# Optimization experiments

Hardware: AMD Instinct MI355X
Metric: run time of the kernel (lower is better)

Reference implementation:

```python
import jax, jax.numpy as jnp
import numpy as np

N_MESH, N_GRID, N_EDGE = 2562, 16384, 49152
D, EDGE_DIM, OUT_DIM = 512, 4, 128
LN_EPS = 1e-5


def _mlp_ln(x, w1, b1, w2, b2, g, beta):
    # Linear -> ReLU -> Linear -> LayerNorm (activate_final=False, use_layer_norm=True)
    h = jax.nn.relu(x @ w1 + b1)
    h = h @ w2 + b2
    mu = jnp.mean(h, axis=-1, keepdims=True)
    var = jnp.var(h, axis=-1, keepdims=True)
    return (h - mu) * jax.lax.rsqrt(var + LN_EPS) * g + beta


def setup_inputs() -> dict:
    key = jax.random.key(0)
    ks = iter(jax.random.split(key, 40))

    def W(i, o):
        return (jax.random.normal(next(ks), (i, o), jnp.float32) / np.float32(np.sqrt(i)))

    inp = {
        "input_mesh_nodes": jax.random.normal(next(ks), (N_MESH, D), jnp.float32),
        "input_grid_nodes": jax.random.normal(next(ks), (N_GRID, D), jnp.float32),
        "input_edge_attr": jax.random.normal(next(ks), (N_EDGE, EDGE_DIM), jnp.float32),
        "edge_index": jnp.stack([
            jax.random.randint(next(ks), (N_EDGE,), 0, N_MESH, jnp.int32),  # senders (mesh)
            jax.random.randint(next(ks), (N_EDGE,), 0, N_GRID, jnp.int32),  # receivers (grid)
        ], axis=0),
        # edges_mlp: EDGE_DIM -> D -> D, LN
        "emlp_w1": W(EDGE_DIM, D), "emlp_b1": jnp.zeros((D,), jnp.float32),
        "emlp_w2": W(D, D), "emlp_b2": jnp.zeros((D,), jnp.float32),
        "emlp_g": jnp.ones((D,), jnp.float32), "emlp_beta": jnp.zeros((D,), jnp.float32),
        # gnn message MLP: 3D -> D -> D, LN   (cat(x_i, x_j, edge_attr))
        "ge_w1": W(3 * D, D), "ge_b1": jnp.zeros((D,), jnp.float32),
        "ge_w2": W(D, D), "ge_b2": jnp.zeros((D,), jnp.float32),
        "ge_g": jnp.ones((D,), jnp.float32), "ge_beta": jnp.zeros((D,), jnp.float32),
        # gnn node MLP: 2D -> D -> D, LN   (cat(receiver_x, aggr))
        "gn_w1": W(2 * D, D), "gn_b1": jnp.zeros((D,), jnp.float32),
        "gn_w2": W(D, D), "gn_b2": jnp.zeros((D,), jnp.float32),
        "gn_g": jnp.ones((D,), jnp.float32), "gn_beta": jnp.zeros((D,), jnp.float32),
        # grid_mlp_final: D -> D -> OUT_DIM, LN
        "fin_w1": W(D, D), "fin_b1": jnp.zeros((D,), jnp.float32),
        "fin_w2": W(D, OUT_DIM), "fin_b2": jnp.zeros((OUT_DIM,), jnp.float32),
        "fin_g": jnp.ones((OUT_DIM,), jnp.float32), "fin_beta": jnp.zeros((OUT_DIM,), jnp.float32),
    }
    return inp


def reference(input_mesh_nodes, input_grid_nodes, input_edge_attr, edge_index,
              emlp_w1, emlp_b1, emlp_w2, emlp_b2, emlp_g, emlp_beta,
              ge_w1, ge_b1, ge_w2, ge_b2, ge_g, ge_beta,
              gn_w1, gn_b1, gn_w2, gn_b2, gn_g, gn_beta,
              fin_w1, fin_b1, fin_w2, fin_b2, fin_g, fin_beta):
    # edge embedding MLP
    edges_emb = _mlp_ln(input_edge_attr, emlp_w1, emlp_b1, emlp_w2, emlp_b2, emlp_g, emlp_beta)
    senders, receivers = edge_index[0], edge_index[1]
    x_i = input_grid_nodes[receivers]   # receiver (grid) features gathered per edge
    x_j = input_mesh_nodes[senders]     # sender (mesh) features gathered per edge
    # per-edge message MLP on cat(x_i, x_j, edge_attr)
    msg = _mlp_ln(jnp.concatenate([x_i, x_j, edges_emb], axis=-1),
                  ge_w1, ge_b1, ge_w2, ge_b2, ge_g, ge_beta)  # [E, D]
    # scatter-add messages to receiver grid nodes (aggr='add')
    aggr = jax.ops.segment_sum(msg, receivers, num_segments=N_GRID)  # [N_GRID, D]
    # node update MLP on cat(receiver_x, aggr)
    gnn_out = _mlp_ln(jnp.concatenate([input_grid_nodes, aggr], axis=-1),
                      gn_w1, gn_b1, gn_w2, gn_b2, gn_g, gn_beta)
    latent_grid_nodes = input_grid_nodes + gnn_out  # residual
    return _mlp_ln(latent_grid_nodes, fin_w1, fin_b1, fin_w2, fin_b2, fin_g, fin_beta)
```

## Files before the change

### kernel.cpp

```cpp
#include <hip/hip_runtime.h>
#include <hip/hip_bf16.h>
#include <stdint.h>

#define LN_EPS 1e-5f

typedef __hip_bfloat16 bf16;
typedef short short8 __attribute__((ext_vector_type(8)));
typedef float f32x4 __attribute__((ext_vector_type(4)));

static __device__ __forceinline__ float bf2f(short s) {
    unsigned int u = ((unsigned int)(unsigned short)s) << 16;
    return __uint_as_float(u);
}
static __device__ __forceinline__ short f2bf(float x) {
    __hip_bfloat16 h = __float2bfloat16(x);
    return *reinterpret_cast<short*>(&h);
}

static __device__ __forceinline__ void gload16(const void* g, void* l) {
    __builtin_amdgcn_global_load_lds((const __attribute__((address_space(1))) void*)g,
                                     (__attribute__((address_space(3))) void*)l, 16, 0, 0);
}

struct TDesc { const float* src; bf16* dst; int K; int N; int kOff; const float* scale; };
struct TDescs { TDesc d[9]; };

__global__ void transpose_all_kernel(TDescs descs) {
    TDesc t = descs.d[blockIdx.z];
    int kb = blockIdx.x * 32, nb = blockIdx.y * 32;
    if (kb >= t.K || nb >= t.N) return;
    __shared__ float tile[32][33];
    int tx = threadIdx.x & 31, ty = threadIdx.x >> 5;
    for (int i = ty; i < 32; i += 8) {
        int k = kb + i, n = nb + tx;
        float v = (k < t.K && n < t.N) ? t.src[(size_t)(t.kOff + k) * t.N + n] : 0.f;
        if (t.scale && k < t.K) v *= t.scale[k];
        tile[i][tx] = v;
    }
    __syncthreads();
    for (int i = ty; i < 32; i += 8) {
        int n = nb + i, k = kb + tx;
        if (n < t.N && k < t.K)
            t.dst[(size_t)n * t.K + k] = __float2bfloat16(tile[tx][i]);
    }
}

__global__ void uv_kernel(const float* __restrict__ W, const float* __restrict__ g,
                          const float* __restrict__ be, float* __restrict__ u,
                          float* __restrict__ v) {
    int n = blockIdx.x * 256 + threadIdx.x;
    if (n >= 512) return;
    float su = 0.f, sv = 0.f;
    for (int k = 0; k < 512; k++) {
        float w = W[(size_t)(1024 + k) * 512 + n];
        su += g[k] * w;
        sv += be[k] * w;
    }
    u[n] = su;
    v[n] = sv;
}

__global__ void cvt_bf16_kernel(const float* __restrict__ src, bf16* __restrict__ dst, int n) {
    int i = blockIdx.x * 256 + threadIdx.x;
    int idx = i * 4;
    if (idx >= n) return;
    float4 v = *(const float4*)(src + idx);
    dst[idx + 0] = __float2bfloat16(v.x);
    dst[idx + 1] = __float2bfloat16(v.y);
    dst[idx + 2] = __float2bfloat16(v.z);
    dst[idx + 3] = __float2bfloat16(v.w);
}

__global__ void edge_l1_kernel(const float* __restrict__ attr, const float* __restrict__ w1,
                               const float* __restrict__ b1, bf16* __restrict__ h1, int E) {
    int e = blockIdx.x * 4 + (threadIdx.x >> 6);
    if (e >= E) return;
    int lane = threadIdx.x & 63;
    int d0 = lane * 8;
    float4 a = *(const float4*)(attr + (size_t)e * 4);
    float av[4] = {a.x, a.y, a.z, a.w};
    float s[8];
    {
        float4 c0 = *(const float4*)(b1 + d0), c1 = *(const float4*)(b1 + d0 + 4);
        s[0]=c0.x; s[1]=c0.y; s[2]=c0.z; s[3]=c0.w; s[4]=c1.x; s[5]=c1.y; s[6]=c1.z; s[7]=c1.w;
    }
#pragma unroll
    for (int k = 0; k < 4; k++) {
        float4 w0 = *(const float4*)(w1 + k * 512 + d0);
        float4 w1v = *(const float4*)(w1 + k * 512 + d0 + 4);
        float wv[8] = {w0.x, w0.y, w0.z, w0.w, w1v.x, w1v.y, w1v.z, w1v.w};
#pragma unroll
        for (int j = 0; j < 8; j++) s[j] += av[k] * wv[j];
    }
    short8 o;
#pragma unroll
    for (int j = 0; j < 8; j++) o[j] = f2bf(fmaxf(s[j], 0.f));
    *(short8*)(h1 + (size_t)e * 512 + d0) = o;
}

template <int EPI>
__global__ __launch_bounds__(512, 4) void gemm256_kernel(
    const bf16* __restrict__ A, const bf16* __restrict__ BT,
    const float* __restrict__ bias, bf16* __restrict__ C, int M, int N, int K,
    const bf16* __restrict__ gridp, const bf16* __restrict__ meshp,
    const int* __restrict__ send, const int* __restrict__ recv,
    const float2* __restrict__ stats, const float* __restrict__ uvec,
    const float* __restrict__ vvec) {
    __shared__ short SMEM[384 * 64];
    const int t = threadIdx.x;
    const int lane = t & 63, w = t >> 6;
    const int wm = w >> 1, wn = w & 1;
    const int lr = lane & 15, lh = lane >> 4;

    int gx = gridDim.x;
    int nwg = gx * gridDim.y;
    int orig = blockIdx.y * gx + blockIdx.x;
    int q = nwg >> 3, r = nwg & 7;
    int xcd = orig & 7, loc = orig >> 3;
    int wg = (xcd < r ? xcd * (q + 1) : r * (q + 1) + (xcd - r) * q) + loc;
    int bx = wg % gx, by = wg / gx;
    const int row0 = by * 256;
    const int col0 = bx * 128;

    const int sr3 = lane >> 3;
    const int su = (lane & 7) ^ sr3;
    const int scol = su * 8;
    const bf16* gp6[6];
#pragma unroll
    for (int i = 0; i < 6; i++) {
        int rr = w * 48 + i * 8 + sr3;
        if (rr < 256) {
            int ra = row0 + rr; if (ra >= M) ra = M - 1;
            gp6[i] = A + (size_t)ra * K + scol;
        } else {
            int rb = col0 + (rr - 256); if (rb >= N) rb = N - 1;
            gp6[i] = BT + (size_t)rb * K + scol;
        }
    }

    f32x4 acc[4][4];
#pragma unroll
    for (int i = 0; i < 4; i++)
#pragma unroll
        for (int j = 0; j < 4; j++) acc[i][j] = {0.f, 0.f, 0.f, 0.f};

    for (int k0 = 0; k0 < K; k0 += 64) {
#pragma unroll
        for (int i = 0; i < 6; i++)
            gload16(gp6[i] + k0, SMEM + (w * 48 + i * 8) * 64);
        __syncthreads();
#pragma unroll
        for (int kk = 0; kk < 64; kk += 32) {
            short8 af[4], bfv[4];
#pragma unroll
            for (int mf = 0; mf < 4; mf++) {
                int rowa = wm * 64 + mf * 16 + lr;
                int ua = ((kk >> 3) + lh) ^ (rowa & 7);
                af[mf] = *(const short8*)&SMEM[rowa * 64 + ua * 8];
            }
#pragma unroll
            for (int nf = 0; nf < 4; nf++) {
                int rowb = 256 + wn * 64 + nf * 16 + lr;
                int ub = ((kk >> 3) + lh) ^ (rowb & 7);
                bfv[nf] = *(const short8*)&SMEM[rowb * 64 + ub * 8];
            }
#pragma unroll
            for (int mf = 0; mf < 4; mf++)
#pragma unroll
                for (int nf = 0; nf < 4; nf++)
                    acc[mf][nf] = __builtin_amdgcn_mfma_f32_16x16x32_bf16(
                        af[mf], bfv[nf], acc[mf][nf], 0, 0, 0);
        }
        __syncthreads();
    }

    short* Cw = SMEM + w * (32 * 66);
    const int rgrp = lane >> 3, u = lane & 7;
#pragma unroll
    for (int hp = 0; hp < 2; hp++) {
#pragma unroll
        for (int mf2 = 0; mf2 < 2; mf2++) {
            int mf = hp * 2 + mf2;
#pragma unroll
            for (int nf = 0; nf < 4; nf++)
#pragma unroll
                for (int r2 = 0; r2 < 4; r2++) {
                    int rl = mf2 * 16 + lh * 4 + r2;
                    Cw[rl * 66 + nf * 16 + lr] = f2bf(acc[mf][nf][r2]);
                }
        }
#pragma unroll
        for (int rr = 0; rr < 4; rr++) {
            int rl = rr * 8 + rgrp;
            int grow = row0 + wm * 64 + hp * 32 + rl;
            int gcol = col0 + wn * 64 + u * 8;
            short8 vv = *(const short8*)&Cw[rl * 66 + u * 8];
            float vf[8];
#pragma unroll
            for (int j = 0; j < 8; j++) vf[j] = bf2f(vv[j]);
            if (EPI == 4) {
                int e = grow < M ? grow : M - 1;
                float2 st = stats[e];
                float rs = st.y, mrs = st.x * st.y;
                float4 u0 = *(const float4*)(uvec + gcol), u1 = *(const float4*)(uvec + gcol + 4);
                float4 v0 = *(const float4*)(vvec + gcol), v1 = *(const float4*)(vvec + gcol + 4);
                float uu[8] = {u0.x, u0.y, u0.z, u0.w, u1.x, u1.y, u1.z, u1.w};
                float vvv[8] = {v0.x, v0.y, v0.z, v0.w, v1.x, v1.y, v1.z, v1.w};
#pragma unroll
                for (int j = 0; j < 8; j++) vf[j] = rs * vf[j] - mrs * uu[j] + vvv[j];
            }
            if (EPI >= 1) {
                float4 c0 = *(const float4*)(bias + gcol);
                float4 c1 = *(const float4*)(bias + gcol + 4);
                float bb[8] = {c0.x, c0.y, c0.z, c0.w, c1.x, c1.y, c1.z, c1.w};
#pragma unroll
                for (int j = 0; j < 8; j++) vf[j] += bb[j];
            }
            if (EPI == 4) {
                int e = grow < M ? grow : M - 1;
                int rn = recv[e], sn = send[e];
                short8 gp = *(const short8*)(gridp + (size_t)rn * 512 + gcol);
                short8 mp = *(const short8*)(meshp + (size_t)sn * 512 + gcol);
#pragma unroll
                for (int j = 0; j < 8; j++) vf[j] += bf2f(gp[j]) + bf2f(mp[j]);
            }
            if (EPI == 2 || EPI == 4) {
#pragma unroll
                for (int j = 0; j < 8; j++) vf[j] = fmaxf(vf[j], 0.f);
            }
            short8 o;
#pragma unroll
            for (int j = 0; j < 8; j++) o[j] = f2bf(vf[j]);
            if (grow < M && gcol < N)
                *(short8*)(C + (size_t)grow * N + gcol) = o;
        }
    }
}

template <int EPI>
__global__ __launch_bounds__(256, 4) void gemm_bt_kernel(
    const bf16* __restrict__ A, const bf16* __restrict__ BT,
    const float* __restrict__ bias, bf16* __restrict__ C, int M, int N, int K,
    const float* __restrict__ fg, const float* __restrict__ fb,
    float* __restrict__ OutF) {
    __shared__ short SMEM[132 * 128 + 64];
    const int t = threadIdx.x;
    const int lane = t & 63, w = t >> 6;
    const int wm = w >> 1, wn = w & 1;
    const int lr = lane & 15, lh = lane >> 4;

    int gx = gridDim.x;
    int nwg = gx * gridDim.y;
    int orig = blockIdx.y * gx + blockIdx.x;
    int q = nwg >> 3, r = nwg & 7;
    int xcd = orig & 7, loc = orig >> 3;
    int wg = (xcd < r ? xcd * (q + 1) : r * (q + 1) + (xcd - r) * q) + loc;
    int bx = wg % gx, by = wg / gx;
    const int row0 = by * 128;
    const int col0 = bx * 128;

    const int sr3 = lane >> 3;
    const int su = (lane & 7) ^ sr3;
    const int srow = w * 32 + sr3;
    const int scol = su * 8;
    const bf16* gaP[4];
    const bf16* gbP[4];
#pragma unroll
    for (int i = 0; i < 4; i++) {
        int ra = row0 + srow + i * 8; if (ra >= M) ra = M - 1;
        int rb = col0 + srow + i * 8; if (rb >= N) rb = N - 1;
        gaP[i] = A + (size_t)ra * K + scol;
        gbP[i] = BT + (size_t)rb * K + scol;
    }

    f32x4 acc[4][4];
#pragma unroll
    for (int i = 0; i < 4; i++)
#pragma unroll
        for (int j = 0; j < 4; j++) acc[i][j] = {0.f, 0.f, 0.f, 0.f};

    for (int k0 = 0; k0 < K; k0 += 64) {
        short* la = SMEM + w * 32 * 64;
        short* lb = la + 8192;
#pragma unroll
        for (int i = 0; i < 4; i++) {
            gload16(gaP[i] + k0, la + i * 8 * 64);
            gload16(gbP[i] + k0, lb + i * 8 * 64);
        }
        __syncthreads();
#pragma unroll
        for (int kk = 0; kk < 64; kk += 32) {
            short8 af[4], bfv[4];
#pragma unroll
            for (int mf = 0; mf < 4; mf++) {
                int rowa = wm * 64 + mf * 16 + lr;
                int ua = ((kk >> 3) + lh) ^ (rowa & 7);
                af[mf] = *(const short8*)&SMEM[rowa * 64 + ua * 8];
            }
#pragma unroll
            for (int nf = 0; nf < 4; nf++) {
                int rowb = wn * 64 + nf * 16 + lr;
                int ub = ((kk >> 3) + lh) ^ (rowb & 7);
                bfv[nf] = *(const short8*)&SMEM[8192 + rowb * 64 + ub * 8];
            }
#pragma unroll
            for (int mf = 0; mf < 4; mf++)
#pragma unroll
                for (int nf = 0; nf < 4; nf++)
                    acc[mf][nf] = __builtin_amdgcn_mfma_f32_16x16x32_bf16(
                        af[mf], bfv[nf], acc[mf][nf], 0, 0, 0);
        }
        __syncthreads();
    }

    if (EPI == 5) {
        short* Cs = SMEM;
#pragma unroll
        for (int nf = 0; nf < 4; nf++) {
            float bv = bias[wn * 64 + nf * 16 + lr];
#pragma unroll
            for (int mf = 0; mf < 4; mf++)
#pragma unroll
                for (int r2 = 0; r2 < 4; r2++) {
                    int rl = wm * 64 + mf * 16 + lh * 4 + r2;
                    Cs[rl * 132 + wn * 64 + nf * 16 + lr] = f2bf(acc[mf][nf][r2] + bv);
                }
        }
        __syncthreads();
        int rl = w * 32 + (lane >> 1);
        int half = lane & 1;
        short8 vs[8];
        float s = 0.f, s2 = 0.f;
#pragma unroll
        for (int j8 = 0; j8 < 8; j8++) {
            vs[j8] = *(const short8*)&Cs[rl * 132 + half * 64 + j8 * 8];
#pragma unroll
            for (int j = 0; j < 8; j++) {
                float f = bf2f(vs[j8][j]);
                s += f; s2 += f * f;
            }
        }
        s += __shfl_xor(s, 1, 64);
        s2 += __shfl_xor(s2, 1, 64);
        float mu = s * (1.f / 128.f);
        float var = s2 * (1.f / 128.f) - mu * mu;
        float rs = rsqrtf(var + LN_EPS);
        int grow = row0 + rl;
#pragma unroll
        for (int j8 = 0; j8 < 8; j8++) {
            int c0 = half * 64 + j8 * 8;
            float4 g0 = *(const float4*)(fg + c0), g1 = *(const float4*)(fg + c0 + 4);
            float4 b0 = *(const float4*)(fb + c0), b1v = *(const float4*)(fb + c0 + 4);
            float gg[8] = {g0.x, g0.y, g0.z, g0.w, g1.x, g1.y, g1.z, g1.w};
            float bb[8] = {b0.x, b0.y, b0.z, b0.w, b1v.x, b1v.y, b1v.z, b1v.w};
            float4 o0, o1;
#pragma unroll
            for (int j = 0; j < 8; j++) {
                float y = (bf2f(vs[j8][j]) - mu) * rs * gg[j] + bb[j];
                if (j < 4) ((float*)&o0)[j] = y; else ((float*)&o1)[j - 4] = y;
            }
            *(float4*)(OutF + (size_t)grow * 128 + c0) = o0;
            *(float4*)(OutF + (size_t)grow * 128 + c0 + 4) = o1;
        }
        return;
    }

    short* Cw = SMEM + w * (32 * 66);
    const int rgrp = lane >> 3, u = lane & 7;
#pragma unroll
    for (int hp = 0; hp < 2; hp++) {
#pragma unroll
        for (int mf2 = 0; mf2 < 2; mf2++) {
            int mf = hp * 2 + mf2;
#pragma unroll
            for (int nf = 0; nf < 4; nf++)
#pragma unroll
                for (int r2 = 0; r2 < 4; r2++) {
                    int rl = mf2 * 16 + lh * 4 + r2;
                    Cw[rl * 66 + nf * 16 + lr] = f2bf(acc[mf][nf][r2]);
                }
        }
#pragma unroll
        for (int rr = 0; rr < 4; rr++) {
            int rl = rr * 8 + rgrp;
            int grow = row0 + wm * 64 + hp * 32 + rl;
            int gcol = col0 + wn * 64 + u * 8;
            short8 vv = *(const short8*)&Cw[rl * 66 + u * 8];
            float vf[8];
#pragma unroll
            for (int j = 0; j < 8; j++) vf[j] = bf2f(vv[j]);
            if (EPI >= 1) {
                float4 c0 = *(const float4*)(bias + gcol);
                float4 c1 = *(const float4*)(bias + gcol + 4);
                float bb[8] = {c0.x, c0.y, c0.z, c0.w, c1.x, c1.y, c1.z, c1.w};
#pragma unroll
                for (int j = 0; j < 8; j++) vf[j] += bb[j];
            }
            if (EPI == 2) {
#pragma unroll
                for (int j = 0; j < 8; j++) vf[j] = fmaxf(vf[j], 0.f);
            }
            short8 o;
#pragma unroll
            for (int j = 0; j < 8; j++) o[j] = f2bf(vf[j]);
            if (grow < M && gcol < N)
                *(short8*)(C + (size_t)grow * N + gcol) = o;
        }
    }
}

__global__ void ln_resid_kernel(const bf16* __restrict__ X, const float* __restrict__ gw,
                                const float* __restrict__ bw, bf16* __restrict__ outb,
                                const bf16* __restrict__ resid, int R) {
    int row = blockIdx.x * 4 + (threadIdx.x >> 6);
    if (row >= R) return;
    int lane = threadIdx.x & 63;
    short8 t8 = *(const short8*)(X + (size_t)row * 512 + lane * 8);
    float v[8];
#pragma unroll
    for (int j = 0; j < 8; j++) v[j] = bf2f(t8[j]);
    float s = 0.f, s2 = 0.f;
#pragma unroll
    for (int j = 0; j < 8; j++) { s += v[j]; s2 += v[j] * v[j]; }
#pragma unroll
    for (int o = 32; o > 0; o >>= 1) {
        s += __shfl_xor(s, o, 64);
        s2 += __shfl_xor(s2, o, 64);
    }
    float mu = s * (1.f / 512.f);
    float var = s2 * (1.f / 512.f) - mu * mu;
    float rs = rsqrtf(var + LN_EPS);
    int d0 = lane * 8;
    short8 rv = *(const short8*)(resid + (size_t)row * 512 + d0);
    short8 o;
#pragma unroll
    for (int j = 0; j < 8; j++) {
        float y = (v[j] - mu) * rs * gw[d0 + j] + bw[d0 + j];
        o[j] = f2bf(bf2f(rv[j]) + y);
    }
    *(short8*)(outb + (size_t)row * 512 + d0) = o;
}

__global__ void ln_stats_kernel(const bf16* __restrict__ X, float2* __restrict__ stats, int R) {
    int row = blockIdx.x * 4 + (threadIdx.x >> 6);
    if (row >= R) return;
    int lane = threadIdx.x & 63;
    short8 t8 = *(const short8*)(X + (size_t)row * 512 + lane * 8);
    float s = 0.f, s2 = 0.f;
#pragma unroll
    for (int j = 0; j < 8; j++) {
        float x = bf2f(t8[j]);
        s += x; s2 += x * x;
    }
#pragma unroll
    for (int o = 32; o > 0; o >>= 1) {
        s += __shfl_xor(s, o, 64);
        s2 += __shfl_xor(s2, o, 64);
    }
    float mu = s * (1.f / 512.f);
    float var = s2 * (1.f / 512.f) - mu * mu;
    if (lane == 0) stats[row] = make_float2(mu, rsqrtf(var + LN_EPS));
}

__global__ void degree_kernel(const int* __restrict__ recv, int* __restrict__ deg, int E) {
    int e = blockIdx.x * 256 + threadIdx.x;
    if (e < E) atomicAdd(&deg[recv[e]], 1);
}

__global__ void scan_kernel(const int* __restrict__ deg, int* __restrict__ off) {
    __shared__ int partial[1024];
    int t = threadIdx.x;
    int base = t * 16;
    int v[16];
    int s = 0;
#pragma unroll
    for (int i = 0; i < 16; i++) { v[i] = deg[base + i]; s += v[i]; }
    partial[t] = s;
    __syncthreads();
    for (int o = 1; o < 1024; o <<= 1) {
        int x = (t >= o) ? partial[t - o] : 0;
        __syncthreads();
        partial[t] += x;
        __syncthreads();
    }
    int run = (t == 0) ? 0 : partial[t - 1];
#pragma unroll
    for (int i = 0; i < 16; i++) { off[base + i] = run; run += v[i]; }
    if (t == 1023) off[16384] = run;
}

__global__ void scatter_kernel(const int* __restrict__ recv, const int* __restrict__ off,
                               int* __restrict__ cnt, int* __restrict__ edges, int E) {
    int e = blockIdx.x * 256 + threadIdx.x;
    if (e < E) {
        int r = recv[e];
        int p = atomicAdd(&cnt[r], 1);
        edges[off[r] + p] = e;
    }
}

__global__ void aggregate_kernel(const bf16* __restrict__ T5, const float2* __restrict__ stats,
                                 const float* __restrict__ gw, const float* __restrict__ bw,
                                 const bf16* __restrict__ gridb,
                                 const int* __restrict__ off, const int* __restrict__ edges,
                                 bf16* __restrict__ X2, int G) {
    int g = blockIdx.x * 4 + (threadIdx.x >> 6);
    if (g >= G) return;
    int lane = threadIdx.x & 63;
    int d0 = lane * 8;
    float gg[8], bb[8];
    {
        float4 a = *(const float4*)(gw + d0), b = *(const float4*)(gw + d0 + 4);
        gg[0]=a.x; gg[1]=a.y; gg[2]=a.z; gg[3]=a.w; gg[4]=b.x; gg[5]=b.y; gg[6]=b.z; gg[7]=b.w;
        float4 c = *(const float4*)(bw + d0), d = *(const float4*)(bw + d0 + 4);
        bb[0]=c.x; bb[1]=c.y; bb[2]=c.z; bb[3]=c.w; bb[4]=d.x; bb[5]=d.y; bb[6]=d.z; bb[7]=d.w;
    }
    float s[8] = {0.f, 0.f, 0.f, 0.f, 0.f, 0.f, 0.f, 0.f};
    int a = off[g], b = off[g + 1];
    for (int i = a; i < b; i++) {
        int e = edges[i];
        float2 st = stats[e];
        short8 m = *(const short8*)(T5 + (size_t)e * 512 + d0);
#pragma unroll
        for (int j = 0; j < 8; j++)
            s[j] += (bf2f(m[j]) - st.x) * st.y * gg[j] + bb[j];
    }
    *(short8*)(X2 + (size_t)g * 1024 + d0) = *(const short8*)(gridb + (size_t)g * 512 + d0);
    short8 o;
#pragma unroll
    for (int j = 0; j < 8; j++) o[j] = f2bf(s[j]);
    *(short8*)(X2 + (size_t)g * 1024 + 512 + d0) = o;
}

extern "C" void kernel_launch(void* const* d_in, const int* in_sizes, int n_in,
                              void* d_out, int out_size, void* d_ws, size_t ws_size,
                              hipStream_t stream) {
    const int NM = 2562, NG = 16384, NE = 49152;
    const float* mesh   = (const float*)d_in[0];
    const float* grid   = (const float*)d_in[1];
    const float* attr   = (const float*)d_in[2];
    const int*   eidx   = (const int*)d_in[3];
    const int*   send   = eidx;
    const int*   recv   = eidx + NE;
    const float* emlp_w1 = (const float*)d_in[4];
    const float* emlp_b1 = (const float*)d_in[5];
    const float* emlp_w2 = (const float*)d_in[6];
    const float* emlp_b2 = (const float*)d_in[7];
    const float* emlp_g  = (const float*)d_in[8];
    const float* emlp_be = (const float*)d_in[9];
    const float* ge_w1 = (const float*)d_in[10];
    const float* ge_b1 = (const float*)d_in[11];
    const float* ge_w2 = (const float*)d_in[12];
    const float* ge_b2 = (const float*)d_in[13];
    const float* ge_g  = (const float*)d_in[14];
    const float* ge_be = (const float*)d_in[15];
    const float* gn_w1 = (const float*)d_in[16];
    const float* gn_b1 = (const float*)d_in[17];
    const float* gn_w2 = (const float*)d_in[18];
    const float* gn_b2 = (const float*)d_in[19];
    const float* gn_g  = (const float*)d_in[20];
    const float* gn_be = (const float*)d_in[21];
    const float* fin_w1 = (const float*)d_in[22];
    const float* fin_b1 = (const float*)d_in[23];
    const float* fin_w2 = (const float*)d_in[24];
    const float* fin_b2 = (const float*)d_in[25];
    const float* fin_g  = (const float*)d_in[26];
    const float* fin_be = (const float*)d_in[27];

    char* p = (char*)d_ws;
    auto take = [&](size_t bytes) -> char* {
        char* r = p;
        p += (bytes + 255) & ~(size_t)255;
        return r;
    };
    bf16* emlp_w2T = (bf16*)take((size_t)512 * 512 * 2);
    bf16* geA_T    = (bf16*)take((size_t)512 * 512 * 2);
    bf16* geB_T    = (bf16*)take((size_t)512 * 512 * 2);
    bf16* geC_T    = (bf16*)take((size_t)512 * 512 * 2);
    bf16* ge_w2T   = (bf16*)take((size_t)512 * 512 * 2);
    bf16* gn_w1T   = (bf16*)take((size_t)512 * 1024 * 2);
    bf16* gn_w2T   = (bf16*)take((size_t)512 * 512 * 2);
    bf16* fin_w1T  = (bf16*)take((size_t)512 * 512 * 2);
    bf16* fin_w2T  = (bf16*)take((size_t)128 * 512 * 2);
    bf16* grid_bf  = (bf16*)take((size_t)NG * 512 * 2);
    bf16* mesh_bf  = (bf16*)take((size_t)NM * 512 * 2);
    bf16* bufA     = (bf16*)take((size_t)NE * 512 * 2);
    bf16* bufB     = (bf16*)take((size_t)NE * 512 * 2);
    bf16* bufC     = (bf16*)take((size_t)NG * 512 * 2);
    bf16* bufD     = (bf16*)take((size_t)NM * 512 * 2);
    float2* stats  = (float2*)take((size_t)NE * 8);
    float* uvecW   = (float*)take((size_t)512 * 4);
    float* vvecW   = (float*)take((size_t)512 * 4);
    int*  deg      = (int*)take((size_t)NG * 4);
    int*  cnt      = (int*)take((size_t)NG * 4);
    int*  csr_off  = (int*)take((size_t)(NG + 1) * 4);
    int*  csr_edge = (int*)take((size_t)NE * 4);

    const bf16* nbf = nullptr; const int* ni = nullptr;
    const float2* nst = nullptr; const float* nf = nullptr;

    TDescs td;
    td.d[0] = {emlp_w2, emlp_w2T, 512, 512, 0, nullptr};
    td.d[1] = {ge_w1,   geA_T,    512, 512, 0, nullptr};
    td.d[2] = {ge_w1,   geB_T,    512, 512, 512, nullptr};
    td.d[3] = {ge_w1,   geC_T,    512, 512, 1024, emlp_g};
    td.d[4] = {ge_w2,   ge_w2T,   512, 512, 0, nullptr};
    td.d[5] = {gn_w1,   gn_w1T,  1024, 512, 0, nullptr};
    td.d[6] = {gn_w2,   gn_w2T,   512, 512, 0, nullptr};
    td.d[7] = {fin_w1,  fin_w1T,  512, 512, 0, nullptr};
    td.d[8] = {fin_w2,  fin_w2T,  512, 128, 0, nullptr};
    hipLaunchKernelGGL(transpose_all_kernel, dim3(32, 16, 9), dim3(256), 0, stream, td);
    hipLaunchKernelGGL(uv_kernel, dim3(2), dim3(256), 0, stream,
                       ge_w1, emlp_g, emlp_be, uvecW, vvecW);

    hipLaunchKernelGGL(cvt_bf16_kernel, dim3((NG * 512 / 4 + 255) / 256), dim3(256), 0, stream,
                       grid, grid_bf, NG * 512);
    hipLaunchKernelGGL(cvt_bf16_kernel, dim3((NM * 512 / 4 + 255) / 256), dim3(256), 0, stream,
                       mesh, mesh_bf, NM * 512);
    hipMemsetAsync(deg, 0, (size_t)NG * 4, stream);
    hipMemsetAsync(cnt, 0, (size_t)NG * 4, stream);
    hipLaunchKernelGGL(degree_kernel, dim3((NE + 255) / 256), dim3(256), 0, stream, recv, deg, NE);
    hipLaunchKernelGGL(scan_kernel, dim3(1), dim3(1024), 0, stream, deg, csr_off);
    hipLaunchKernelGGL(scatter_kernel, dim3((NE + 255) / 256), dim3(256), 0, stream,
                       recv, csr_off, cnt, csr_edge, NE);

    hipLaunchKernelGGL(edge_l1_kernel, dim3(NE / 4), dim3(256), 0, stream,
                       attr, emlp_w1, emlp_b1, bufA, NE);
    hipLaunchKernelGGL(gemm256_kernel<1>, dim3(4, NE / 256), dim3(512), 0, stream,
                       bufA, emlp_w2T, emlp_b2, bufB, NE, 512, 512,
                       nbf, nbf, ni, ni, nst, nf, nf);
    hipLaunchKernelGGL(ln_stats_kernel, dim3(NE / 4), dim3(256), 0, stream, bufB, stats, NE);

    hipLaunchKernelGGL(gemm_bt_kernel<0>, dim3(4, NG / 128), dim3(256), 0, stream,
                       grid_bf, geA_T, nf, bufC, NG, 512, 512, nf, nf, (float*)nullptr);
    hipLaunchKernelGGL(gemm_bt_kernel<0>, dim3(4, (NM + 127) / 128), dim3(256), 0, stream,
                       mesh_bf, geB_T, nf, bufD, NM, 512, 512, nf, nf, (float*)nullptr);
    hipLaunchKernelGGL(gemm256_kernel<4>, dim3(4, NE / 256), dim3(512), 0, stream,
                       bufB, geC_T, ge_b1, bufA, NE, 512, 512,
                       bufC, bufD, send, recv, stats, uvecW, vvecW);
    hipLaunchKernelGGL(gemm256_kernel<1>, dim3(4, NE / 256), dim3(512), 0, stream,
                       bufA, ge_w2T, ge_b2, bufB, NE, 512, 512,
                       nbf, nbf, ni, ni, nst, nf, nf);
    hipLaunchKernelGGL(ln_stats_kernel, dim3(NE / 4), dim3(256), 0, stream, bufB, stats, NE);
    hipLaunchKernelGGL(aggregate_kernel, dim3(NG / 4), dim3(256), 0, stream,
                       bufB, stats, ge_g, ge_be, grid_bf, csr_off, csr_edge, bufA, NG);

    hipLaunchKernelGGL(gemm_bt_kernel<2>, dim3(4, NG / 128), dim3(256), 0, stream,
                       bufA, gn_w1T, gn_b1, bufC, NG, 512, 1024, nf, nf, (float*)nullptr);
    hipLaunchKernelGGL(gemm_bt_kernel<1>, dim3(4, NG / 128), dim3(256), 0, stream,
                       bufC, gn_w2T, gn_b2, bufB, NG, 512, 512, nf, nf, (float*)nullptr);
    hipLaunchKernelGGL(ln_resid_kernel, dim3(NG / 4), dim3(256), 0, stream,
                       bufB, gn_g, gn_be, bufA, grid_bf, NG);

    hipLaunchKernelGGL(gemm_bt_kernel<2>, dim3(4, NG / 128), dim3(256), 0, stream,
                       bufA, fin_w1T, fin_b1, bufC, NG, 512, 512, nf, nf, (float*)nullptr);
    hipLaunchKernelGGL(gemm_bt_kernel<5>, dim3(1, NG / 128), dim3(256), 0, stream,
                       bufC, fin_w2T, fin_b2, (bf16*)nullptr, NG, 128, 512,
                       fin_g, fin_be, (float*)d_out);
}
```

Baseline: 358.2 us.

## Fuse edge layer-1 into GEMM and compute LayerNorm partial stats in epilogue

The edge embedding's first layer (4->512, ReLU) now runs inside the second-layer GEMM: each block builds its A tile in LDS from the raw edge attributes instead of reading a materialized h1 buffer. The GEMM epilogues also emit per-row partial sums and sums of squares, which a small finalize kernel reduces. This replaces the separate ln_stats passes that re-read the E×512 outputs. The cost is redundant layer-1 compute across the 4 column blocks, only B being async-loaded, and stats now taken from fp32 values before bf16 rounding.

```diff
diff --git a/kernel.cpp b/kernel.cpp
--- a/kernel.cpp
+++ b/kernel.cpp
@@ -71,41 +71,26 @@
     dst[idx + 3] = __float2bfloat16(v.w);
 }
 
-__global__ void edge_l1_kernel(const float* __restrict__ attr, const float* __restrict__ w1,
-                               const float* __restrict__ b1, bf16* __restrict__ h1, int E) {
-    int e = blockIdx.x * 4 + (threadIdx.x >> 6);
-    if (e >= E) return;
-    int lane = threadIdx.x & 63;
-    int d0 = lane * 8;
-    float4 a = *(const float4*)(attr + (size_t)e * 4);
-    float av[4] = {a.x, a.y, a.z, a.w};
-    float s[8];
-    {
-        float4 c0 = *(const float4*)(b1 + d0), c1 = *(const float4*)(b1 + d0 + 4);
-        s[0]=c0.x; s[1]=c0.y; s[2]=c0.z; s[3]=c0.w; s[4]=c1.x; s[5]=c1.y; s[6]=c1.z; s[7]=c1.w;
-    }
-#pragma unroll
-    for (int k = 0; k < 4; k++) {
-        float4 w0 = *(const float4*)(w1 + k * 512 + d0);
-        float4 w1v = *(const float4*)(w1 + k * 512 + d0 + 4);
-        float wv[8] = {w0.x, w0.y, w0.z, w0.w, w1v.x, w1v.y, w1v.z, w1v.w};
-#pragma unroll
-        for (int j = 0; j < 8; j++) s[j] += av[k] * wv[j];
-    }
-    short8 o;
-#pragma unroll
-    for (int j = 0; j < 8; j++) o[j] = f2bf(fmaxf(s[j], 0.f));
-    *(short8*)(h1 + (size_t)e * 512 + d0) = o;
-}
-
-template <int EPI>
-__global__ __launch_bounds__(512, 4) void gemm256_kernel(
-    const bf16* __restrict__ A, const bf16* __restrict__ BT,
-    const float* __restrict__ bias, bf16* __restrict__ C, int M, int N, int K,
-    const bf16* __restrict__ gridp, const bf16* __restrict__ meshp,
-    const int* __restrict__ send, const int* __restrict__ recv,
-    const float2* __restrict__ stats, const float* __restrict__ uvec,
-    const float* __restrict__ vvec) {
+__global__ void stats_finalize_kernel(const float2* __restrict__ partials,
+                                      float2* __restrict__ stats, int R) {
+    int r = blockIdx.x * 256 + threadIdx.x;
+    if (r >= R) return;
+    float s = 0.f, q = 0.f;
+#pragma unroll
+    for (int i = 0; i < 8; i++) {
+        float2 pp = partials[(size_t)r * 8 + i];
+        s += pp.x; q += pp.y;
+    }
+    float mu = s * (1.f / 512.f);
+    float var = q * (1.f / 512.f) - mu * mu;
+    stats[r] = make_float2(mu, rsqrtf(var + LN_EPS));
+}
+
+__global__ __launch_bounds__(512, 4) void t2_fused_kernel(
+    const float* __restrict__ attr, const float* __restrict__ w1,
+    const float* __restrict__ b1, const bf16* __restrict__ BT,
+    const float* __restrict__ bias, bf16* __restrict__ C,
+    float2* __restrict__ partials, int M, int N, int K) {
     __shared__ short SMEM[384 * 64];
     const int t = threadIdx.x;
     const int lane = t & 63, w = t >> 6;
@@ -122,6 +107,156 @@
     const int row0 = by * 256;
     const int col0 = bx * 128;
 
+    const int cg = t & 7;
+    const int rowblk = t >> 3;
+    float av[4][4];
+#pragma unroll
+    for (int rr = 0; rr < 4; rr++) {
+        int e = row0 + rowblk * 4 + rr; if (e >= M) e = M - 1;
+        float4 a = *(const float4*)(attr + (size_t)e * 4);
+        av[rr][0] = a.x; av[rr][1] = a.y; av[rr][2] = a.z; av[rr][3] = a.w;
+    }
+
+    const int sr3 = lane >> 3;
+    const int su = (lane & 7) ^ sr3;
+    const int scol = su * 8;
+    const bf16* gbP[2];
+#pragma unroll
+    for (int c = 0; c < 2; c++) {
+        int rb = col0 + w * 16 + c * 8 + sr3; if (rb >= N) rb = N - 1;
+        gbP[c] = BT + (size_t)rb * K + scol;
+    }
+
+    f32x4 acc[4][4];
+#pragma unroll
+    for (int i = 0; i < 4; i++)
+#pragma unroll
+        for (int j = 0; j < 4; j++) acc[i][j] = {0.f, 0.f, 0.f, 0.f};
+
+    for (int k0 = 0; k0 < K; k0 += 64) {
+#pragma unroll
+        for (int c = 0; c < 2; c++)
+            gload16(gbP[c] + k0, SMEM + (256 + w * 16 + c * 8) * 64);
+        int kc = k0 + cg * 8;
+        float4 bb0 = *(const float4*)(b1 + kc);
+        float4 bb1 = *(const float4*)(b1 + kc + 4);
+        float wv[4][8];
+#pragma unroll
+        for (int j2 = 0; j2 < 4; j2++) {
+            float4 w0 = *(const float4*)(w1 + j2 * 512 + kc);
+            float4 w1v = *(const float4*)(w1 + j2 * 512 + kc + 4);
+            wv[j2][0] = w0.x; wv[j2][1] = w0.y; wv[j2][2] = w0.z; wv[j2][3] = w0.w;
+            wv[j2][4] = w1v.x; wv[j2][5] = w1v.y; wv[j2][6] = w1v.z; wv[j2][7] = w1v.w;
+        }
+#pragma unroll
+        for (int rr = 0; rr < 4; rr++) {
+            int row = rowblk * 4 + rr;
+            float c8[8] = {bb0.x, bb0.y, bb0.z, bb0.w, bb1.x, bb1.y, bb1.z, bb1.w};
+#pragma unroll
+            for (int j2 = 0; j2 < 4; j2++)
+#pragma unroll
+                for (int j = 0; j < 8; j++) c8[j] += av[rr][j2] * wv[j2][j];
+            short8 h;
+#pragma unroll
+            for (int j = 0; j < 8; j++) h[j] = f2bf(fmaxf(c8[j], 0.f));
+            *(short8*)&SMEM[row * 64 + ((cg ^ (row & 7)) * 8)] = h;
+        }
+        __syncthreads();
+#pragma unroll
+        for (int kk = 0; kk < 64; kk += 32) {
+            short8 af[4], bfv[4];
+#pragma unroll
+            for (int mf = 0; mf < 4; mf++) {
+                int rowa = wm * 64 + mf * 16 + lr;
+                int ua = ((kk >> 3) + lh) ^ (rowa & 7);
+                af[mf] = *(const short8*)&SMEM[rowa * 64 + ua * 8];
+            }
+#pragma unroll
+            for (int nf = 0; nf < 4; nf++) {
+                int rowb = 256 + wn * 64 + nf * 16 + lr;
+                int ub = ((kk >> 3) + lh) ^ (rowb & 7);
+                bfv[nf] = *(const short8*)&SMEM[rowb * 64 + ub * 8];
+            }
+#pragma unroll
+            for (int mf = 0; mf < 4; mf++)
+#pragma unroll
+                for (int nf = 0; nf < 4; nf++)
+                    acc[mf][nf] = __builtin_amdgcn_mfma_f32_16x16x32_bf16(
+                        af[mf], bfv[nf], acc[mf][nf], 0, 0, 0);
+        }
+        __syncthreads();
+    }
+
+    short* Cw = SMEM + w * (32 * 66);
+    const int rgrp = lane >> 3, u = lane & 7;
+#pragma unroll
+    for (int hp = 0; hp < 2; hp++) {
+#pragma unroll
+        for (int mf2 = 0; mf2 < 2; mf2++) {
+            int mf = hp * 2 + mf2;
+#pragma unroll
+            for (int nf = 0; nf < 4; nf++)
+#pragma unroll
+                for (int r2 = 0; r2 < 4; r2++) {
+                    int rl = mf2 * 16 + lh * 4 + r2;
+                    Cw[rl * 66 + nf * 16 + lr] = f2bf(acc[mf][nf][r2]);
+                }
+        }
+#pragma unroll
+        for (int rr = 0; rr < 4; rr++) {
+            int rl = rr * 8 + rgrp;
+            int grow = row0 + wm * 64 + hp * 32 + rl;
+            int gcol = col0 + wn * 64 + u * 8;
+            short8 vv = *(const short8*)&Cw[rl * 66 + u * 8];
+            float vf[8];
+#pragma unroll
+            for (int j = 0; j < 8; j++) vf[j] = bf2f(vv[j]);
+            float4 c0 = *(const float4*)(bias + gcol);
+            float4 c1 = *(const float4*)(bias + gcol + 4);
+            float bb[8] = {c0.x, c0.y, c0.z, c0.w, c1.x, c1.y, c1.z, c1.w};
+#pragma unroll
+            for (int j = 0; j < 8; j++) vf[j] += bb[j];
+            float s1 = 0.f, s2 = 0.f;
+#pragma unroll
+            for (int j = 0; j < 8; j++) { s1 += vf[j]; s2 += vf[j] * vf[j]; }
+            s1 += __shfl_xor(s1, 1, 64); s2 += __shfl_xor(s2, 1, 64);
+            s1 += __shfl_xor(s1, 2, 64); s2 += __shfl_xor(s2, 2, 64);
+            s1 += __shfl_xor(s1, 4, 64); s2 += __shfl_xor(s2, 4, 64);
+            if (u == 0 && grow < M)
+                partials[(size_t)grow * 8 + bx * 2 + wn] = make_float2(s1, s2);
+            short8 o;
+#pragma unroll
+            for (int j = 0; j < 8; j++) o[j] = f2bf(vf[j]);
+            if (grow < M && gcol < N)
+                *(short8*)(C + (size_t)grow * N + gcol) = o;
+        }
+    }
+}
+
+template <int EPI, int STATS>
+__global__ __launch_bounds__(512, 4) void gemm256_kernel(
+    const bf16* __restrict__ A, const bf16* __restrict__ BT,
+    const float* __restrict__ bias, bf16* __restrict__ C, int M, int N, int K,
+    const bf16* __restrict__ gridp, const bf16* __restrict__ meshp,
+    const int* __restrict__ send, const int* __restrict__ recv,
+    const float2* __restrict__ stats, const float* __restrict__ uvec,
+    const float* __restrict__ vvec, float2* __restrict__ partials) {
+    __shared__ short SMEM[384 * 64];
+    const int t = threadIdx.x;
+    const int lane = t & 63, w = t >> 6;
+    const int wm = w >> 1, wn = w & 1;
+    const int lr = lane & 15, lh = lane >> 4;
+
+    int gx = gridDim.x;
+    int nwg = gx * gridDim.y;
+    int orig = blockIdx.y * gx + blockIdx.x;
+    int q = nwg >> 3, r = nwg & 7;
+    int xcd = orig & 7, loc = orig >> 3;
+    int wg = (xcd < r ? xcd * (q + 1) : r * (q + 1) + (xcd - r) * q) + loc;
+    int bx = wg % gx, by = wg / gx;
+    const int row0 = by * 256;
+    const int col0 = bx * 128;
+
     const int sr3 = lane >> 3;
     const int su = (lane & 7) ^ sr3;
     const int scol = su * 8;
@@ -209,7 +344,7 @@
 #pragma unroll
                 for (int j = 0; j < 8; j++) vf[j] = rs * vf[j] - mrs * uu[j] + vvv[j];
             }
-            if (EPI >= 1) {
+            {
                 float4 c0 = *(const float4*)(bias + gcol);
                 float4 c1 = *(const float4*)(bias + gcol + 4);
                 float bb[8] = {c0.x, c0.y, c0.z, c0.w, c1.x, c1.y, c1.z, c1.w};
@@ -223,10 +358,18 @@
                 short8 mp = *(const short8*)(meshp + (size_t)sn * 512 + gcol);
 #pragma unroll
                 for (int j = 0; j < 8; j++) vf[j] += bf2f(gp[j]) + bf2f(mp[j]);
-            }
-            if (EPI == 2 || EPI == 4) {
 #pragma unroll
                 for (int j = 0; j < 8; j++) vf[j] = fmaxf(vf[j], 0.f);
+            }
+            if (STATS) {
+                float s1 = 0.f, s2 = 0.f;
+#pragma unroll
+                for (int j = 0; j < 8; j++) { s1 += vf[j]; s2 += vf[j] * vf[j]; }
+                s1 += __shfl_xor(s1, 1, 64); s2 += __shfl_xor(s2, 1, 64);
+                s1 += __shfl_xor(s1, 2, 64); s2 += __shfl_xor(s2, 2, 64);
+                s1 += __shfl_xor(s1, 4, 64); s2 += __shfl_xor(s2, 4, 64);
+                if (u == 0 && grow < M)
+                    partials[(size_t)grow * 8 + bx * 2 + wn] = make_float2(s1, s2);
             }
             short8 o;
 #pragma unroll
@@ -439,27 +582,6 @@
         o[j] = f2bf(bf2f(rv[j]) + y);
     }
     *(short8*)(outb + (size_t)row * 512 + d0) = o;
-}
-
-__global__ void ln_stats_kernel(const bf16* __restrict__ X, float2* __restrict__ stats, int R) {
-    int row = blockIdx.x * 4 + (threadIdx.x >> 6);
-    if (row >= R) return;
-    int lane = threadIdx.x & 63;
-    short8 t8 = *(const short8*)(X + (size_t)row * 512 + lane * 8);
-    float s = 0.f, s2 = 0.f;
-#pragma unroll
-    for (int j = 0; j < 8; j++) {
-        float x = bf2f(t8[j]);
-        s += x; s2 += x * x;
-    }
-#pragma unroll
-    for (int o = 32; o > 0; o >>= 1) {
-        s += __shfl_xor(s, o, 64);
-        s2 += __shfl_xor(s2, o, 64);
-    }
-    float mu = s * (1.f / 512.f);
-    float var = s2 * (1.f / 512.f) - mu * mu;
-    if (lane == 0) stats[row] = make_float2(mu, rsqrtf(var + LN_EPS));
 }
 
 __global__ void degree_kernel(const int* __restrict__ recv, int* __restrict__ deg, int E) {
@@ -589,6 +711,7 @@
     bf16* bufC     = (bf16*)take((size_t)NG * 512 * 2);
     bf16* bufD     = (bf16*)take((size_t)NM * 512 * 2);
     float2* stats  = (float2*)take((size_t)NE * 8);
+    float2* parts  = (float2*)take((size_t)NE * 8 * 8);
     float* uvecW   = (float*)take((size_t)512 * 4);
     float* vvecW   = (float*)take((size_t)512 * 4);
     int*  deg      = (int*)take((size_t)NG * 4);
@@ -598,6 +721,7 @@
 
     const bf16* nbf = nullptr; const int* ni = nullptr;
     const float2* nst = nullptr; const float* nf = nullptr;
+    float2* nfp = nullptr;
 
     TDescs td;
     td.d[0] = {emlp_w2, emlp_w2T, 512, 512, 0, nullptr};
@@ -624,24 +748,23 @@
     hipLaunchKernelGGL(scatter_kernel, dim3((NE + 255) / 256), dim3(256), 0, stream,
                        recv, csr_off, cnt, csr_edge, NE);
 
-    hipLaunchKernelGGL(edge_l1_kernel, dim3(NE / 4), dim3(256), 0, stream,
-                       attr, emlp_w1, emlp_b1, bufA, NE);
-    hipLaunchKernelGGL(gemm256_kernel<1>, dim3(4, NE / 256), dim3(512), 0, stream,
-                       bufA, emlp_w2T, emlp_b2, bufB, NE, 512, 512,
-                       nbf, nbf, ni, ni, nst, nf, nf);
-    hipLaunchKernelGGL(ln_stats_kernel, dim3(NE / 4), dim3(256), 0, stream, bufB, stats, NE);
+    hipLaunchKernelGGL(t2_fused_kernel, dim3(4, NE / 256), dim3(512), 0, stream,
+                       attr, emlp_w1, emlp_b1, emlp_w2T, emlp_b2, bufB, parts, NE, 512, 512);
+    hipLaunchKernelGGL(stats_finalize_kernel, dim3((NE + 255) / 256), dim3(256), 0, stream,
+                       parts, stats, NE);
 
     hipLaunchKernelGGL(gemm_bt_kernel<0>, dim3(4, NG / 128), dim3(256), 0, stream,
                        grid_bf, geA_T, nf, bufC, NG, 512, 512, nf, nf, (float*)nullptr);
     hipLaunchKernelGGL(gemm_bt_kernel<0>, dim3(4, (NM + 127) / 128), dim3(256), 0, stream,
                        mesh_bf, geB_T, nf, bufD, NM, 512, 512, nf, nf, (float*)nullptr);
-    hipLaunchKernelGGL(gemm256_kernel<4>, dim3(4, NE / 256), dim3(512), 0, stream,
+    hipLaunchKernelGGL((gemm256_kernel<4, 0>), dim3(4, NE / 256), dim3(512), 0, stream,
                        bufB, geC_T, ge_b1, bufA, NE, 512, 512,
-                       bufC, bufD, send, recv, stats, uvecW, vvecW);
-    hipLaunchKernelGGL(gemm256_kernel<1>, dim3(4, NE / 256), dim3(512), 0, stream,
+                       bufC, bufD, send, recv, stats, uvecW, vvecW, nfp);
+    hipLaunchKernelGGL((gemm256_kernel<1, 1>), dim3(4, NE / 256), dim3(512), 0, stream,
                        bufA, ge_w2T, ge_b2, bufB, NE, 512, 512,
-                       nbf, nbf, ni, ni, nst, nf, nf);
-    hipLaunchKernelGGL(ln_stats_kernel, dim3(NE / 4), dim3(256), 0, stream, bufB, stats, NE);
+                       nbf, nbf, ni, ni, nst, nf, nf, parts);
+    hipLaunchKernelGGL(stats_finalize_kernel, dim3((NE + 255) / 256), dim3(256), 0, stream,
+                       parts, stats, NE);
     hipLaunchKernelGGL(aggregate_kernel, dim3(NG / 4), dim3(256), 0, stream,
                        bufB, stats, ge_g, ge_be, grid_bf, csr_off, csr_edge, bufA, NG);
 
```

Measured after the change: 405.6 us. 13.2% more time.
